# Performance work log

Hardware: AMD Instinct MI355X
Metric: run time of the kernel (lower is better)

## Reference

```python
import jax, jax.numpy as jnp
import numpy as np

N_NODES = 50000
N_ROWS = 800000  # total rows across all k-hop neighborhoods (sum_i |N_i|)
C_IN = 128
C_OUT = 128


def setup_inputs() -> dict:
    key = jax.random.key(0)
    k1, k2, k3, k4 = jax.random.split(key, 4)
    x = jax.random.normal(k1, (N_NODES, C_IN), dtype=jnp.float32)
    nbr_idx = jax.random.randint(k2, (N_ROWS,), 0, N_NODES, dtype=jnp.int64)
    W1 = jax.random.normal(k3, (2 * C_IN, C_IN), dtype=jnp.float32) * (1.0 / np.sqrt(2 * C_IN))
    b1 = jnp.zeros((C_IN,), dtype=jnp.float32)
    W2 = jax.random.normal(k4, (C_IN, C_OUT), dtype=jnp.float32) * (1.0 / np.sqrt(C_IN))
    b2 = jnp.zeros((C_OUT,), dtype=jnp.float32)
    return {"x": x, "nbr_idx": nbr_idx, "W1": W1, "b1": b1, "W2": W2, "b2": b2}


def reference(x, nbr_idx, W1, b1, W2, b2):
    # transfer1 to k-hop neighborhoods: with singleton source domains both
    # first-order linmap components are a gather of x[node], concatenated -> 2*C channels.
    g = x[nbr_idx]                              # [E, C] irregular gather
    h = jnp.concatenate([g, g], axis=-1)        # [E, 2C]
    h = jax.nn.relu(h @ W1 + b1)                # lin1 + relu
    # dropout in eval mode (identity) for a deterministic reference
    y = h @ W2 + b2                             # lin2
    return y
```

## Files before the change

kernel.cpp:

```cpp
#include <hip/hip_runtime.h>

typedef float v4f __attribute__((ext_vector_type(4)));

#define N_NODES 50000
#define N_ROWS  800000
#define C 128

__global__ __launch_bounds__(256) void prep_w1f(const float* __restrict__ W1,
                                                float* __restrict__ W1f) {
    int i = blockIdx.x * 256 + threadIdx.x;
    if (i < C * C) W1f[i] = W1[i] + W1[C * C + i];
}

__global__ __launch_bounds__(256) void node_kernel(
    const float* __restrict__ x, const float* __restrict__ W1f,
    const float* __restrict__ b1, const float* __restrict__ W2,
    const float* __restrict__ b2, float* __restrict__ z)
{
    __shared__ float smem[64 * 132];
    const int tid = threadIdx.x;
    const int cg  = tid & 15;
    const int rg  = tid >> 4;
    const int c0  = cg * 8;
    const int node0 = blockIdx.x * 64;

    {
        int r  = tid >> 5;
        int c4 = (tid & 31) * 4;
        #pragma unroll
        for (int it = 0; it < 8; ++it, r += 8) {
            int gr = node0 + r;
            if (gr >= N_NODES) gr = N_NODES - 1;
            v4f v = *reinterpret_cast<const v4f*>(&x[(long)gr * C + c4]);
            *reinterpret_cast<v4f*>(&smem[r * 132 + c4]) = v;
        }
    }
    __syncthreads();

    float acc[4][8];
    #pragma unroll
    for (int m = 0; m < 4; ++m)
        #pragma unroll
        for (int j = 0; j < 8; ++j) acc[m][j] = 0.f;

    #pragma unroll 4
    for (int k = 0; k < C; ++k) {
        v4f w0 = *reinterpret_cast<const v4f*>(&W1f[k * C + c0]);
        v4f w1 = *reinterpret_cast<const v4f*>(&W1f[k * C + c0 + 4]);
        #pragma unroll
        for (int m = 0; m < 4; ++m) {
            float xv = smem[(rg + 16 * m) * 132 + k];
            acc[m][0] += xv * w0.x; acc[m][1] += xv * w0.y;
            acc[m][2] += xv * w0.z; acc[m][3] += xv * w0.w;
            acc[m][4] += xv * w1.x; acc[m][5] += xv * w1.y;
            acc[m][6] += xv * w1.z; acc[m][7] += xv * w1.w;
        }
    }

    float bb[8];
    #pragma unroll
    for (int j = 0; j < 8; ++j) bb[j] = b1[c0 + j];

    __syncthreads();
    #pragma unroll
    for (int m = 0; m < 4; ++m) {
        int r = rg + 16 * m;
        v4f h0, h1;
        h0.x = acc[m][0] + bb[0]; h0.y = acc[m][1] + bb[1];
        h0.z = acc[m][2] + bb[2]; h0.w = acc[m][3] + bb[3];
        h1.x = acc[m][4] + bb[4]; h1.y = acc[m][5] + bb[5];
        h1.z = acc[m][6] + bb[6]; h1.w = acc[m][7] + bb[7];
        h0.x = h0.x > 0.f ? h0.x : 0.f; h0.y = h0.y > 0.f ? h0.y : 0.f;
        h0.z = h0.z > 0.f ? h0.z : 0.f; h0.w = h0.w > 0.f ? h0.w : 0.f;
        h1.x = h1.x > 0.f ? h1.x : 0.f; h1.y = h1.y > 0.f ? h1.y : 0.f;
        h1.z = h1.z > 0.f ? h1.z : 0.f; h1.w = h1.w > 0.f ? h1.w : 0.f;
        *reinterpret_cast<v4f*>(&smem[r * 132 + c0])     = h0;
        *reinterpret_cast<v4f*>(&smem[r * 132 + c0 + 4]) = h1;
    }
    __syncthreads();

    #pragma unroll
    for (int m = 0; m < 4; ++m)
        #pragma unroll
        for (int j = 0; j < 8; ++j) acc[m][j] = 0.f;

    #pragma unroll 4
    for (int k = 0; k < C; ++k) {
        v4f w0 = *reinterpret_cast<const v4f*>(&W2[k * C + c0]);
        v4f w1 = *reinterpret_cast<const v4f*>(&W2[k * C + c0 + 4]);
        #pragma unroll
        for (int m = 0; m < 4; ++m) {
            float hv = smem[(rg + 16 * m) * 132 + k];
            acc[m][0] += hv * w0.x; acc[m][1] += hv * w0.y;
            acc[m][2] += hv * w0.z; acc[m][3] += hv * w0.w;
            acc[m][4] += hv * w1.x; acc[m][5] += hv * w1.y;
            acc[m][6] += hv * w1.z; acc[m][7] += hv * w1.w;
        }
    }

    #pragma unroll
    for (int j = 0; j < 8; ++j) bb[j] = b2[c0 + j];

    #pragma unroll
    for (int m = 0; m < 4; ++m) {
        int gr = node0 + rg + 16 * m;
        if (gr < N_NODES) {
            v4f o0, o1;
            o0.x = acc[m][0] + bb[0]; o0.y = acc[m][1] + bb[1];
            o0.z = acc[m][2] + bb[2]; o0.w = acc[m][3] + bb[3];
            o1.x = acc[m][4] + bb[4]; o1.y = acc[m][5] + bb[5];
            o1.z = acc[m][6] + bb[6]; o1.w = acc[m][7] + bb[7];
            *reinterpret_cast<v4f*>(&z[(long)gr * C + c0])     = o0;
            *reinterpret_cast<v4f*>(&z[(long)gr * C + c0 + 4]) = o1;
        }
    }
}

__global__ __launch_bounds__(256) void gather_kernel(
    const v4f* __restrict__ z4, const int* __restrict__ idx,
    v4f* __restrict__ y4)
{
    long i = (long)blockIdx.x * 256 + threadIdx.x;
    int row = (int)(i >> 5);
    int c   = (int)(i & 31);
    int n = idx[row];
    v4f v = z4[(long)n * 32 + c];
    __builtin_nontemporal_store(v, &y4[i]);
}

extern "C" void kernel_launch(void* const* d_in, const int* in_sizes, int n_in,
                              void* d_out, int out_size, void* d_ws, size_t ws_size,
                              hipStream_t stream) {
    const float* x   = (const float*)d_in[0];
    const int*   idx = (const int*)d_in[1];
    const float* W1  = (const float*)d_in[2];
    const float* b1  = (const float*)d_in[3];
    const float* W2  = (const float*)d_in[4];
    const float* b2  = (const float*)d_in[5];
    float* y = (float*)d_out;

    float* z   = (float*)d_ws;
    float* W1f = z + (size_t)N_NODES * C;

    hipLaunchKernelGGL(prep_w1f, dim3(64), dim3(256), 0, stream, W1, W1f);
    hipLaunchKernelGGL(node_kernel, dim3((N_NODES + 63) / 64), dim3(256), 0, stream,
                       x, W1f, b1, W2, b2, z);
    hipLaunchKernelGGL(gather_kernel, dim3((N_ROWS * 32) / 256), dim3(256), 0, stream,
                       (const v4f*)z, idx, (v4f*)y);
}
```

Measured before the change: 541.1 us.

## Sort edge rows by node via counting sort before copying node outputs

```diff
diff --git a/kernel.cpp b/kernel.cpp
--- a/kernel.cpp
+++ b/kernel.cpp
@@ -5,6 +5,8 @@
 #define N_NODES 50000
 #define N_ROWS  800000
 #define C 128
+#define NPAD 50176
+#define NBLK 196
 
 __global__ __launch_bounds__(256) void prep_w1f(const float* __restrict__ W1,
                                                 float* __restrict__ W1f) {
@@ -116,16 +118,79 @@
     }
 }
 
-__global__ __launch_bounds__(256) void gather_kernel(
-    const v4f* __restrict__ z4, const int* __restrict__ idx,
+
+__global__ __launch_bounds__(256) void zero_counts(int* __restrict__ counts) {
+    int i = blockIdx.x * 256 + threadIdx.x;
+    if (i < NPAD) counts[i] = 0;
+}
+
+__global__ __launch_bounds__(256) void hist_kernel(const int* __restrict__ idx,
+                                                   int* __restrict__ counts) {
+    int e = blockIdx.x * 256 + threadIdx.x;
+    if (e < N_ROWS) atomicAdd(&counts[idx[e]], 1);
+}
+
+__global__ __launch_bounds__(256) void scan1(const int* __restrict__ counts,
+                                             int* __restrict__ bases,
+                                             int* __restrict__ partials) {
+    __shared__ int s[256];
+    int b = blockIdx.x, t = threadIdx.x, i = b * 256 + t;
+    int v = (i < N_NODES) ? counts[i] : 0;
+    s[t] = v; __syncthreads();
+    #pragma unroll
+    for (int off = 1; off < 256; off <<= 1) {
+        int u = (t >= off) ? s[t - off] : 0;
+        __syncthreads();
+        s[t] += u;
+        __syncthreads();
+    }
+    bases[i] = s[t] - v;
+    if (t == 255) partials[b] = s[t];
+}
+
+__global__ __launch_bounds__(256) void scan2(const int* __restrict__ bases,
+                                             const int* __restrict__ partials,
+                                             int* __restrict__ cursor) {
+    __shared__ int s[256];
+    __shared__ int ex[256];
+    int b = blockIdx.x, t = threadIdx.x;
+    int v = (t < NBLK) ? partials[t] : 0;
+    s[t] = v; __syncthreads();
+    #pragma unroll
+    for (int off = 1; off < 256; off <<= 1) {
+        int u = (t >= off) ? s[t - off] : 0;
+        __syncthreads();
+        s[t] += u;
+        __syncthreads();
+    }
+    ex[t] = s[t] - v;
+    __syncthreads();
+    int offset = ex[b];
+    int i = b * 256 + t;
+    cursor[i] = bases[i] + offset;
+}
+
+__global__ __launch_bounds__(256) void csr_fill(const int* __restrict__ idx,
+                                                int* __restrict__ cursor,
+                                                int2* __restrict__ elist) {
+    int e = blockIdx.x * 256 + threadIdx.x;
+    if (e < N_ROWS) {
+        int n = idx[e];
+        int pos = atomicAdd(&cursor[n], 1);
+        elist[pos] = make_int2(e, n);
+    }
+}
+
+__global__ __launch_bounds__(256) void scatter_kernel(
+    const v4f* __restrict__ z4, const int2* __restrict__ elist,
     v4f* __restrict__ y4)
 {
     long i = (long)blockIdx.x * 256 + threadIdx.x;
-    int row = (int)(i >> 5);
-    int c   = (int)(i & 31);
-    int n = idx[row];
-    v4f v = z4[(long)n * 32 + c];
-    __builtin_nontemporal_store(v, &y4[i]);
+    int slot = (int)(i >> 5);
+    int c    = (int)(i & 31);
+    int2 en  = elist[slot];
+    v4f v = z4[(long)en.y * 32 + c];
+    __builtin_nontemporal_store(v, &y4[(long)en.x * 32 + c]);
 }
 
 extern "C" void kernel_launch(void* const* d_in, const int* in_sizes, int n_in,
@@ -139,12 +204,24 @@
     const float* b2  = (const float*)d_in[5];
     float* y = (float*)d_out;
 
-    float* z   = (float*)d_ws;
-    float* W1f = z + (size_t)N_NODES * C;
+    float* z        = (float*)d_ws;
+    float* W1f      = z + (size_t)N_NODES * C;
+    int*   counts   = (int*)(W1f + C * C);
+    int*   bases    = counts + NPAD;
+    int*   cursor   = bases + NPAD;
+    int*   partials = cursor + NPAD;
+    int2*  elist    = (int2*)(partials + 256);
 
     hipLaunchKernelGGL(prep_w1f, dim3(64), dim3(256), 0, stream, W1, W1f);
     hipLaunchKernelGGL(node_kernel, dim3((N_NODES + 63) / 64), dim3(256), 0, stream,
                        x, W1f, b1, W2, b2, z);
-    hipLaunchKernelGGL(gather_kernel, dim3((N_ROWS * 32) / 256), dim3(256), 0, stream,
-                       (const v4f*)z, idx, (v4f*)y);
-}
+    hipLaunchKernelGGL(zero_counts, dim3(NBLK), dim3(256), 0, stream, counts);
+    hipLaunchKernelGGL(hist_kernel, dim3((N_ROWS + 255) / 256), dim3(256), 0, stream,
+                       idx, counts);
+    hipLaunchKernelGGL(scan1, dim3(NBLK), dim3(256), 0, stream, counts, bases, partials);
+    hipLaunchKernelGGL(scan2, dim3(NBLK), dim3(256), 0, stream, bases, partials, cursor);
+    hipLaunchKernelGGL(csr_fill, dim3((N_ROWS + 255) / 256), dim3(256), 0, stream,
+                       idx, cursor, elist);
+    hipLaunchKernelGGL(scatter_kernel, dim3((N_ROWS * 32) / 256), dim3(256), 0, stream,
+                       (const v4f*)z, elist, (v4f*)y);
+}
```

New measurement: 598.8 us. 10.7% more time.
